# Kernel tuning notes

Hardware: AMD Instinct MI355X
Metric: run time of the kernel (lower is better)

Reference implementation:

```python
import jax, jax.numpy as jnp
import numpy as np

# Config constants (mirror Qwen3_5TextConfig)
H = 1024        # hidden_size
I = 512         # moe_intermediate_size
IS = 2048       # shared_expert_intermediate_size
E = 16          # num_experts
TOP_K = 4       # num_experts_per_tok
NORM_TOPK = True
B, S = 1, 1024


def setup_inputs() -> dict:
    key = jax.random.key(0)
    ks = jax.random.split(key, 10)
    s = 0.02
    return {
        "hidden_states": jax.random.normal(ks[0], (B, S, H), jnp.float32),
        "w_router": (jax.random.normal(ks[1], (H, E), jnp.float32) * s),
        # stacked expert weights; Linear(H->I) stored as [E, H, I] for einsum
        "w_gate": (jax.random.normal(ks[2], (E, H, I), jnp.float32) * s),
        "w_up": (jax.random.normal(ks[3], (E, H, I), jnp.float32) * s),
        "w_down": (jax.random.normal(ks[4], (E, I, H), jnp.float32) * s),
        # shared expert (dense MLP)
        "ws_gate": (jax.random.normal(ks[5], (H, IS), jnp.float32) * s),
        "ws_up": (jax.random.normal(ks[6], (H, IS), jnp.float32) * s),
        "ws_down": (jax.random.normal(ks[7], (IS, H), jnp.float32) * s),
        "w_shared_gate": (jax.random.normal(ks[8], (H, 1), jnp.float32) * s),
    }


def reference(hidden_states, w_router, w_gate, w_up, w_down,
              ws_gate, ws_up, ws_down, w_shared_gate):
    b, sl, hd = hidden_states.shape
    x = hidden_states.reshape(-1, hd)              # [T, H]
    T = x.shape[0]

    # --- router: softmax in fp32, top-k, optional renormalization ---
    router_logits = x @ w_router                   # [T, E]
    probs = jax.nn.softmax(router_logits.astype(jnp.float32), axis=-1)
    top_w, top_i = jax.lax.top_k(probs, TOP_K)     # [T, K]
    if NORM_TOPK:
        top_w = top_w / top_w.sum(axis=-1, keepdims=True)
    # dense per-token expert weights (zeros off the top-k)
    dense_w = jnp.zeros((T, E), x.dtype).at[jnp.arange(T)[:, None], top_i].set(
        top_w.astype(x.dtype))                     # [T, E]

    # --- expert MLPs (SwiGLU), computed for all experts then masked-combined ---
    g = jnp.einsum('th,ehi->tei', x, w_gate)       # [T, E, I]
    u = jnp.einsum('th,ehi->tei', x, w_up)         # [T, E, I]
    expert_out = jnp.einsum('tei,eih->teh', jax.nn.silu(g) * u, w_down)  # [T, E, H]
    moe_out = jnp.einsum('te,teh->th', dense_w, expert_out)             # [T, H]

    # --- shared expert + sigmoid gate ---
    shared = (jax.nn.silu(x @ ws_gate) * (x @ ws_up)) @ ws_down          # [T, H]
    shared_gate = jax.nn.sigmoid(x @ w_shared_gate)                      # [T, 1]
    out = (moe_out + shared_gate * shared).reshape(b, sl, hd)
    return out, router_logits
```

## Files before the change

### kernel.cpp

```cpp
#include <hip/hip_runtime.h>
#include <hip/hip_bf16.h>

#define T_ 1024
#define H_ 1024
#define I_ 512
#define IS_ 2048
#define E_ 16

typedef __attribute__((ext_vector_type(8))) short short8;
typedef __attribute__((ext_vector_type(4))) float f32x4;

__device__ __forceinline__ unsigned short f2bf(float f) {
  unsigned u = __builtin_bit_cast(unsigned, f);
  unsigned r = (u + 0x7fffu + ((u >> 16) & 1u)) >> 16;
  return (unsigned short)r;
}

__device__ __forceinline__ void gload16(const void* g, void* l) {
  __builtin_amdgcn_global_load_lds(
      (const __attribute__((address_space(1))) unsigned int*)g,
      (__attribute__((address_space(3))) unsigned int*)l, 16, 0, 0);
}

__device__ __forceinline__ void transpose_tile(
    const float* __restrict__ src, unsigned short* __restrict__ dst,
    int C, int dld, long sbs, long dbs, int bx, int by, int bz) {
  __shared__ unsigned short tile[64 * 72];
  const float* s = src + (long)bz * sbs + ((long)by * 64) * C + bx * 64;
  int cgrp = threadIdx.x & 15, rgrp = threadIdx.x >> 4;
  int c = cgrp << 2, r0 = rgrp << 2;
  const float* sp = s + (long)r0 * C + c;
  float4 v0 = *(const float4*)(sp);
  float4 v1 = *(const float4*)(sp + C);
  float4 v2 = *(const float4*)(sp + 2 * C);
  float4 v3 = *(const float4*)(sp + 3 * C);
  ushort4 w;
  w = (ushort4){f2bf(v0.x), f2bf(v1.x), f2bf(v2.x), f2bf(v3.x)};
  *(ushort4*)&tile[(c + 0) * 72 + r0] = w;
  w = (ushort4){f2bf(v0.y), f2bf(v1.y), f2bf(v2.y), f2bf(v3.y)};
  *(ushort4*)&tile[(c + 1) * 72 + r0] = w;
  w = (ushort4){f2bf(v0.z), f2bf(v1.z), f2bf(v2.z), f2bf(v3.z)};
  *(ushort4*)&tile[(c + 2) * 72 + r0] = w;
  w = (ushort4){f2bf(v0.w), f2bf(v1.w), f2bf(v2.w), f2bf(v3.w)};
  *(ushort4*)&tile[(c + 3) * 72 + r0] = w;
  __syncthreads();
  int orr = threadIdx.x >> 2;
  int ks = (threadIdx.x & 3) << 4;
  uint4 o0 = *(const uint4*)&tile[orr * 72 + ks];
  uint4 o1 = *(const uint4*)&tile[orr * 72 + ks + 8];
  unsigned short* d = dst + (long)bz * dbs + (long)(bx * 64 + orr) * dld + by * 64 + ks;
  *(uint4*)d = o0;
  *(uint4*)(d + 8) = o1;
}

__global__ __launch_bounds__(256) void k_pre(
    const float* __restrict__ x, const float* __restrict__ wr,
    const float* __restrict__ wshg,
    const float* __restrict__ wg, const float* __restrict__ wu,
    const float* __restrict__ wd, const float* __restrict__ wsg,
    const float* __restrict__ wsu, const float* __restrict__ wsd,
    unsigned short* __restrict__ xb, float* __restrict__ logits_out,
    int* __restrict__ top_i, float* __restrict__ top_w, float* __restrict__ gate_sig,
    unsigned short* __restrict__ WGUT, unsigned short* __restrict__ WDT,
    unsigned short* __restrict__ WSGUT, unsigned short* __restrict__ WSDT) {
  __shared__ float red[4][17];
  int id = blockIdx.x;
  if (id >= T_) {
    id -= T_;
    if (id < 4096) {
      const float* s = id < 2048 ? wg : wu;
      unsigned short* dd = id < 2048 ? WGUT : WGUT + (size_t)I_ * H_;
      int l = id & 2047;
      int bz = l >> 7, r = l & 127;
      transpose_tile(s, dd, I_, H_, (long)H_ * I_, (long)2 * I_ * H_, r & 7, r >> 3, bz);
    } else if (id < 6144) {
      int l = id - 4096;
      int bz = l >> 7, r = l & 127;
      transpose_tile(wd, WDT, H_, I_, (long)I_ * H_, (long)H_ * I_, r & 15, r >> 4, bz);
    } else if (id < 7168) {
      int l = id - 6144;
      const float* s = l < 512 ? wsg : wsu;
      unsigned short* dd = l < 512 ? WSGUT : WSGUT + (size_t)IS_ * H_;
      l &= 511;
      transpose_tile(s, dd, IS_, H_, 0, 0, l & 31, l >> 5, 0);
    } else {
      int l = id - 7168;
      transpose_tile(wsd, WSDT, H_, IS_, 0, 0, l & 15, l >> 4, 0);
    }
    return;
  }
  int t = id, tid = threadIdx.x;
  int h0 = tid << 2;
  float acc[17];
#pragma unroll
  for (int e = 0; e < 17; e++) acc[e] = 0.f;
  float4 xv = *(const float4*)(x + (long)t * H_ + h0);
  float4 wsh = *(const float4*)(wshg + h0);
  ushort4 xo;
  xo.x = f2bf(xv.x); xo.y = f2bf(xv.y); xo.z = f2bf(xv.z); xo.w = f2bf(xv.w);
  *(ushort4*)(xb + (long)t * H_ + h0) = xo;
  float xs[4] = {xv.x, xv.y, xv.z, xv.w};
  float ws[4] = {wsh.x, wsh.y, wsh.z, wsh.w};
#pragma unroll
  for (int j = 0; j < 4; j++) {
    const float4* w4 = (const float4*)(wr + (long)(h0 + j) * 16);
    float4 w0 = w4[0], w1 = w4[1], w2 = w4[2], w3 = w4[3];
    float xvj = xs[j];
    acc[0] += xvj * w0.x; acc[1] += xvj * w0.y; acc[2] += xvj * w0.z; acc[3] += xvj * w0.w;
    acc[4] += xvj * w1.x; acc[5] += xvj * w1.y; acc[6] += xvj * w1.z; acc[7] += xvj * w1.w;
    acc[8] += xvj * w2.x; acc[9] += xvj * w2.y; acc[10] += xvj * w2.z; acc[11] += xvj * w2.w;
    acc[12] += xvj * w3.x; acc[13] += xvj * w3.y; acc[14] += xvj * w3.z; acc[15] += xvj * w3.w;
    acc[16] += xvj * ws[j];
  }
#pragma unroll
  for (int off = 32; off >= 1; off >>= 1) {
#pragma unroll
    for (int e = 0; e < 17; e++) acc[e] += __shfl_xor(acc[e], off, 64);
  }
  int wid = tid >> 6, lane = tid & 63;
  if (lane == 0) {
#pragma unroll
    for (int e = 0; e < 17; e++) red[wid][e] = acc[e];
  }
  __syncthreads();
  if (tid == 0) {
    float a[17];
#pragma unroll
    for (int e = 0; e < 17; e++)
      a[e] = red[0][e] + red[1][e] + red[2][e] + red[3][e];
    float m = a[0];
#pragma unroll
    for (int e = 1; e < 16; e++) m = fmaxf(m, a[e]);
    float p[16], s = 0.f;
#pragma unroll
    for (int e = 0; e < 16; e++) { p[e] = expf(a[e] - m); s += p[e]; }
    float inv = 1.f / s;
#pragma unroll
    for (int e = 0; e < 16; e++) p[e] *= inv;
    int ti[4]; float tw[4]; float tsum = 0.f;
#pragma unroll
    for (int k = 0; k < 4; k++) {
      float best = -1.f; int bi = 0;
#pragma unroll
      for (int e = 0; e < 16; e++)
        if (p[e] > best) { best = p[e]; bi = e; }
      ti[k] = bi; tw[k] = best; tsum += best; p[bi] = -2.f;
    }
    float rn = 1.f / tsum;
#pragma unroll
    for (int e = 0; e < 16; e++) logits_out[(long)t * 16 + e] = a[e];
#pragma unroll
    for (int k = 0; k < 4; k++) {
      top_i[t * 4 + k] = ti[k];
      top_w[t * 4 + k] = tw[k] * rn;
    }
    gate_sig[t] = 1.f / (1.f + expf(-a[16]));
  }
}

__global__ __launch_bounds__(256) void k_build(
    const int* __restrict__ top_i, int* __restrict__ counts,
    int* __restrict__ offsets, int* __restrict__ perm, int* __restrict__ slot_of) {
  __shared__ int cnt[E_], cur[E_];
  int tid = threadIdx.x;
  if (tid < E_) cnt[tid] = 0;
  __syncthreads();
  for (int i = tid; i < T_ * 4; i += 256)
    atomicAdd(&cnt[top_i[i]], 1);
  __syncthreads();
  if (tid == 0) {
    int run = 0;
    for (int e = 0; e < E_; e++) {
      int c = cnt[e];
      counts[e] = c;
      offsets[e] = run;
      cur[e] = run;
      run += c;
    }
  }
  __syncthreads();
  for (int i = tid; i < T_ * 4; i += 256) {
    int e = top_i[i];
    int pos = atomicAdd(&cur[e], 1);
    perm[pos] = i >> 2;
    slot_of[i] = pos;
  }
}

__global__ __launch_bounds__(256) void k_gemm_gu(
    const unsigned short* __restrict__ XB,
    const unsigned short* __restrict__ WSGUT, const unsigned short* __restrict__ WGUT,
    unsigned short* __restrict__ HSB, unsigned short* __restrict__ HB,
    const int* __restrict__ counts, const int* __restrict__ offsets,
    const int* __restrict__ perm) {
  int z = blockIdx.z;
  int mtile = blockIdx.y * 64;
  int ntile = blockIdx.x * 128;
  int M, row_base, uoff, ldd;
  const unsigned short* B0;
  unsigned short* DST;
  const int* pp;
  if (z == 0) {
    M = T_; row_base = 0; B0 = WSGUT; uoff = IS_;
    DST = HSB; ldd = IS_; pp = nullptr;
  } else {
    if (ntile >= I_) return;
    int e = z - 1;
    M = counts[e];
    if (mtile >= M) return;
    row_base = offsets[e];
    B0 = WGUT + (long)e * 2 * I_ * H_;
    uoff = I_;
    DST = HB; ldd = I_; pp = perm;
  }

  __shared__ unsigned short lds[2][10240];

  int tid = threadIdx.x, wid = tid >> 6, lane = tid & 63;
  int sub = lane >> 2;
  int ksw = ((lane & 3) ^ ((sub >> 1) & 3)) << 3;

  int rm = mtile + wid * 16 + sub;
  if (rm > M - 1) rm = M - 1;
  long arow = pp ? (long)pp[row_base + rm] : (long)(row_base + rm);
  const unsigned short* aptr = XB + arow * H_ + ksw;
  int a_off = wid * 512;

  const unsigned short* bgptr[2];
  const unsigned short* buptr[2];
  int b_off[2];
#pragma unroll
  for (int q = 0; q < 2; q++) {
    int r = ntile + q * 64 + wid * 16 + sub;
    bgptr[q] = B0 + (long)r * H_ + ksw;
    buptr[q] = B0 + (long)(r + uoff) * H_ + ksw;
    b_off[q] = q * 2048 + wid * 512;
  }

  int fr = lane & 15, quad = lane >> 4;
  int fslot = (quad ^ ((fr >> 1) & 3)) << 3;
  int wm = (wid >> 1) * 32, wn = (wid & 1) * 64;

  f32x4 acc[2][2][4];
#pragma unroll
  for (int h = 0; h < 2; h++)
#pragma unroll
    for (int i = 0; i < 2; i++)
#pragma unroll
      for (int j = 0; j < 4; j++) acc[h][i][j] = (f32x4){0.f, 0.f, 0.f, 0.f};

  const int NK = H_ / 32;
  gload16(aptr, &lds[0][a_off]);
  gload16(bgptr[0], &lds[0][2048 + b_off[0]]);
  gload16(bgptr[1], &lds[0][2048 + b_off[1]]);
  gload16(buptr[0], &lds[0][6144 + b_off[0]]);
  gload16(buptr[1], &lds[0][6144 + b_off[1]]);

  for (int kt = 0; kt < NK; kt++) {
    int cur = kt & 1;
    __syncthreads();
    if (kt + 1 < NK) {
      int nxt = cur ^ 1, ko = (kt + 1) * 32;
      gload16(aptr + ko, &lds[nxt][a_off]);
      gload16(bgptr[0] + ko, &lds[nxt][2048 + b_off[0]]);
      gload16(bgptr[1] + ko, &lds[nxt][2048 + b_off[1]]);
      gload16(buptr[0] + ko, &lds[nxt][6144 + b_off[0]]);
      gload16(buptr[1] + ko, &lds[nxt][6144 + b_off[1]]);
    }
    const unsigned short* As = &lds[cur][0];
    const unsigned short* Bg = &lds[cur][2048];
    const unsigned short* Bu = &lds[cur][6144];
    short8 af[2], bg[4], bu[4];
#pragma unroll
    for (int i = 0; i < 2; i++)
      af[i] = *(const short8*)(&As[(wm + i * 16 + fr) * 32 + fslot]);
#pragma unroll
    for (int j = 0; j < 4; j++) {
      bg[j] = *(const short8*)(&Bg[(wn + j * 16 + fr) * 32 + fslot]);
      bu[j] = *(const short8*)(&Bu[(wn + j * 16 + fr) * 32 + fslot]);
    }
#pragma unroll
    for (int i = 0; i < 2; i++)
#pragma unroll
      for (int j = 0; j < 4; j++) {
        acc[0][i][j] = __builtin_amdgcn_mfma_f32_16x16x32_bf16(af[i], bg[j], acc[0][i][j], 0, 0, 0);
        acc[1][i][j] = __builtin_amdgcn_mfma_f32_16x16x32_bf16(af[i], bu[j], acc[1][i][j], 0, 0, 0);
      }
  }

#pragma unroll
  for (int i = 0; i < 2; i++) {
    int m0 = mtile + wm + i * 16 + quad * 4;
#pragma unroll
    for (int j = 0; j < 4; j++) {
      int col = ntile + wn + j * 16 + fr;
#pragma unroll
      for (int r = 0; r < 4; r++) {
        int m = m0 + r;
        if (m < M) {
          float g = acc[0][i][j][r], u = acc[1][i][j][r];
          DST[(long)(row_base + m) * ldd + col] = f2bf(g / (1.f + expf(-g)) * u);
        }
      }
    }
  }
}

__global__ __launch_bounds__(256) void k_gemm_dn(
    const unsigned short* __restrict__ HSB, const unsigned short* __restrict__ WSDT,
    float* __restrict__ SHOUT,
    const unsigned short* __restrict__ HB, const unsigned short* __restrict__ WDT,
    float* __restrict__ YD,
    const int* __restrict__ counts, const int* __restrict__ offsets) {
  int z = blockIdx.z;
  int mtile = blockIdx.y * 64;
  int ntile = blockIdx.x * 128;
  const unsigned short *A, *B;
  int K, M, rb;
  float* Y;
  if (z == 0) {
    A = HSB; K = IS_; M = T_; rb = 0; B = WSDT; Y = SHOUT;
  } else {
    int e = z - 1;
    M = counts[e];
    if (mtile >= M) return;
    rb = offsets[e];
    A = HB; K = I_; B = WDT + (long)e * H_ * I_; Y = YD;
  }

  __shared__ unsigned short lds[2][6144];

  int tid = threadIdx.x, wid = tid >> 6, lane = tid & 63;
  int sub = lane >> 2;
  int ksw = ((lane & 3) ^ ((sub >> 1) & 3)) << 3;

  int rm = mtile + wid * 16 + sub;
  if (rm > M - 1) rm = M - 1;
  const unsigned short* aptr = A + (long)(rb + rm) * K + ksw;
  int a_off = wid * 512;

  const unsigned short* bptr[2];
  int b_off[2];
#pragma unroll
  for (int q = 0; q < 2; q++) {
    int r = ntile + q * 64 + wid * 16 + sub;
    bptr[q] = B + (long)r * K + ksw;
    b_off[q] = q * 2048 + wid * 512;
  }

  int fr = lane & 15, quad = lane >> 4;
  int fslot = (quad ^ ((fr >> 1) & 3)) << 3;
  int wm = (wid >> 1) * 32, wn = (wid & 1) * 64;

  f32x4 acc[2][4];
#pragma unroll
  for (int i = 0; i < 2; i++)
#pragma unroll
    for (int j = 0; j < 4; j++) acc[i][j] = (f32x4){0.f, 0.f, 0.f, 0.f};

  const int NK = K / 32;
  gload16(aptr, &lds[0][a_off]);
  gload16(bptr[0], &lds[0][2048 + b_off[0]]);
  gload16(bptr[1], &lds[0][2048 + b_off[1]]);

  for (int kt = 0; kt < NK; kt++) {
    int cur = kt & 1;
    __syncthreads();
    if (kt + 1 < NK) {
      int nxt = cur ^ 1, ko = (kt + 1) * 32;
      gload16(aptr + ko, &lds[nxt][a_off]);
      gload16(bptr[0] + ko, &lds[nxt][2048 + b_off[0]]);
      gload16(bptr[1] + ko, &lds[nxt][2048 + b_off[1]]);
    }
    const unsigned short* As = &lds[cur][0];
    const unsigned short* Bs = &lds[cur][2048];
    short8 af[2], bf[4];
#pragma unroll
    for (int i = 0; i < 2; i++)
      af[i] = *(const short8*)(&As[(wm + i * 16 + fr) * 32 + fslot]);
#pragma unroll
    for (int j = 0; j < 4; j++)
      bf[j] = *(const short8*)(&Bs[(wn + j * 16 + fr) * 32 + fslot]);
#pragma unroll
    for (int i = 0; i < 2; i++)
#pragma unroll
      for (int j = 0; j < 4; j++)
        acc[i][j] = __builtin_amdgcn_mfma_f32_16x16x32_bf16(af[i], bf[j], acc[i][j], 0, 0, 0);
  }

#pragma unroll
  for (int i = 0; i < 2; i++) {
    int m0 = mtile + wm + i * 16 + quad * 4;
#pragma unroll
    for (int j = 0; j < 4; j++) {
      int col = ntile + wn + j * 16 + fr;
#pragma unroll
      for (int r = 0; r < 4; r++) {
        int m = m0 + r;
        if (m < M) Y[(long)(rb + m) * H_ + col] = acc[i][j][r];
      }
    }
  }
}

__global__ __launch_bounds__(256) void k_combine(
    const float* __restrict__ Yd, const float* __restrict__ shout,
    const float* __restrict__ gate_sig, const float* __restrict__ top_w,
    const int* __restrict__ slot_of, float* __restrict__ out) {
  int t = blockIdx.x;
  int c = threadIdx.x << 2;
  float4 sh = *(const float4*)(shout + (long)t * H_ + c);
  float gs = gate_sig[t];
  float4 o;
  o.x = gs * sh.x; o.y = gs * sh.y; o.z = gs * sh.z; o.w = gs * sh.w;
#pragma unroll
  for (int k = 0; k < 4; k++) {
    int s = slot_of[t * 4 + k];
    float w = top_w[t * 4 + k];
    float4 v = *(const float4*)(Yd + (long)s * H_ + c);
    o.x += w * v.x; o.y += w * v.y; o.z += w * v.z; o.w += w * v.w;
  }
  *(float4*)(out + (long)t * H_ + c) = o;
}

extern "C" void kernel_launch(void* const* d_in, const int* in_sizes, int n_in,
                              void* d_out, int out_size, void* d_ws, size_t ws_size,
                              hipStream_t stream) {
  const float* x    = (const float*)d_in[0];
  const float* wrt  = (const float*)d_in[1];
  const float* wg   = (const float*)d_in[2];
  const float* wu   = (const float*)d_in[3];
  const float* wd   = (const float*)d_in[4];
  const float* wsg  = (const float*)d_in[5];
  const float* wsu  = (const float*)d_in[6];
  const float* wsd  = (const float*)d_in[7];
  const float* wshg = (const float*)d_in[8];
  float* out = (float*)d_out;
  float* logits_out = out + (long)T_ * H_;

  char* ws = (char*)d_ws;
  size_t off = 0;
  auto take = [&](size_t bytes) -> void* {
    void* p = ws + off;
    off += (bytes + 255) & ~(size_t)255;
    return p;
  };

  unsigned short* XB    = (unsigned short*)take((size_t)T_ * H_ * 2);
  unsigned short* WGUT  = (unsigned short*)take((size_t)E_ * 2 * I_ * H_ * 2);
  unsigned short* WDT   = (unsigned short*)take((size_t)E_ * H_ * I_ * 2);
  unsigned short* WSGUT = (unsigned short*)take((size_t)2 * IS_ * H_ * 2);
  unsigned short* WSDT  = (unsigned short*)take((size_t)H_ * IS_ * 2);
  float*          YD    = (float*)take((size_t)4096 * H_ * 4);
  unsigned short* HSB   = (unsigned short*)take((size_t)T_ * IS_ * 2);
  float*          SHOUT = (float*)take((size_t)T_ * H_ * 4);
  unsigned short* HB    = (unsigned short*)take((size_t)4096 * I_ * 2);
  int*   counts   = (int*)take(64);
  int*   offsets  = (int*)take(64);
  int*   top_i    = (int*)take((size_t)T_ * 4 * 4);
  float* top_w    = (float*)take((size_t)T_ * 4 * 4);
  int*   perm     = (int*)take((size_t)4096 * 4);
  int*   slot_of  = (int*)take((size_t)4096 * 4);
  float* gate_sig = (float*)take((size_t)T_ * 4);

  k_pre<<<8704, 256, 0, stream>>>(x, wrt, wshg, wg, wu, wd, wsg, wsu, wsd,
                                  XB, logits_out, top_i, top_w, gate_sig,
                                  WGUT, WDT, WSGUT, WSDT);
  k_build<<<1, 256, 0, stream>>>(top_i, counts, offsets, perm, slot_of);

  k_gemm_gu<<<dim3(16, 16, 17), 256, 0, stream>>>(XB, WSGUT, WGUT, HSB, HB,
                                                  counts, offsets, perm);
  k_gemm_dn<<<dim3(8, 16, 17), 256, 0, stream>>>(HSB, WSDT, SHOUT, HB, WDT, YD,
                                                 counts, offsets);
  k_combine<<<T_, 256, 0, stream>>>(YD, SHOUT, gate_sig, top_w, slot_of, out);
}
```

Measured before the change: 287.9 us.

## Halve GEMM N-tile to 64 and use explicit waitcnt/barrier pipelining

```diff
diff --git a/kernel.cpp b/kernel.cpp
--- a/kernel.cpp
+++ b/kernel.cpp
@@ -195,7 +195,7 @@
     const int* __restrict__ perm) {
   int z = blockIdx.z;
   int mtile = blockIdx.y * 64;
-  int ntile = blockIdx.x * 128;
+  int ntile = blockIdx.x * 64;
   int M, row_base, uoff, ldd;
   const unsigned short* B0;
   unsigned short* DST;
@@ -214,7 +214,7 @@
     DST = HB; ldd = I_; pp = perm;
   }
 
-  __shared__ unsigned short lds[2][10240];
+  __shared__ unsigned short lds[2][6144];
 
   int tid = threadIdx.x, wid = tid >> 6, lane = tid & 63;
   int sub = lane >> 2;
@@ -224,75 +224,70 @@
   if (rm > M - 1) rm = M - 1;
   long arow = pp ? (long)pp[row_base + rm] : (long)(row_base + rm);
   const unsigned short* aptr = XB + arow * H_ + ksw;
-  int a_off = wid * 512;
-
-  const unsigned short* bgptr[2];
-  const unsigned short* buptr[2];
-  int b_off[2];
-#pragma unroll
-  for (int q = 0; q < 2; q++) {
-    int r = ntile + q * 64 + wid * 16 + sub;
-    bgptr[q] = B0 + (long)r * H_ + ksw;
-    buptr[q] = B0 + (long)(r + uoff) * H_ + ksw;
-    b_off[q] = q * 2048 + wid * 512;
-  }
+  int rbn = ntile + wid * 16 + sub;
+  const unsigned short* bgptr = B0 + (long)rbn * H_ + ksw;
+  const unsigned short* buptr = B0 + (long)(rbn + uoff) * H_ + ksw;
+  int soff = wid * 512;
 
   int fr = lane & 15, quad = lane >> 4;
   int fslot = (quad ^ ((fr >> 1) & 3)) << 3;
-  int wm = (wid >> 1) * 32, wn = (wid & 1) * 64;
-
-  f32x4 acc[2][2][4];
+  int wm = (wid >> 1) * 32, wn = (wid & 1) * 32;
+
+  f32x4 acc[2][2][2];
 #pragma unroll
   for (int h = 0; h < 2; h++)
 #pragma unroll
     for (int i = 0; i < 2; i++)
 #pragma unroll
-      for (int j = 0; j < 4; j++) acc[h][i][j] = (f32x4){0.f, 0.f, 0.f, 0.f};
+      for (int j = 0; j < 2; j++) acc[h][i][j] = (f32x4){0.f, 0.f, 0.f, 0.f};
 
   const int NK = H_ / 32;
-  gload16(aptr, &lds[0][a_off]);
-  gload16(bgptr[0], &lds[0][2048 + b_off[0]]);
-  gload16(bgptr[1], &lds[0][2048 + b_off[1]]);
-  gload16(buptr[0], &lds[0][6144 + b_off[0]]);
-  gload16(buptr[1], &lds[0][6144 + b_off[1]]);
+  gload16(aptr, &lds[0][soff]);
+  gload16(bgptr, &lds[0][2048 + soff]);
+  gload16(buptr, &lds[0][4096 + soff]);
 
   for (int kt = 0; kt < NK; kt++) {
     int cur = kt & 1;
-    __syncthreads();
     if (kt + 1 < NK) {
-      int nxt = cur ^ 1, ko = (kt + 1) * 32;
-      gload16(aptr + ko, &lds[nxt][a_off]);
-      gload16(bgptr[0] + ko, &lds[nxt][2048 + b_off[0]]);
-      gload16(bgptr[1] + ko, &lds[nxt][2048 + b_off[1]]);
-      gload16(buptr[0] + ko, &lds[nxt][6144 + b_off[0]]);
-      gload16(buptr[1] + ko, &lds[nxt][6144 + b_off[1]]);
-    }
+      int ko = (kt + 1) * 32;
+      gload16(aptr + ko, &lds[cur ^ 1][soff]);
+      gload16(bgptr + ko, &lds[cur ^ 1][2048 + soff]);
+      gload16(buptr + ko, &lds[cur ^ 1][4096 + soff]);
+      asm volatile("s_waitcnt vmcnt(3)" ::: "memory");
+    } else {
+      asm volatile("s_waitcnt vmcnt(0)" ::: "memory");
+    }
+    __builtin_amdgcn_s_barrier();
+    __builtin_amdgcn_sched_barrier(0);
     const unsigned short* As = &lds[cur][0];
     const unsigned short* Bg = &lds[cur][2048];
-    const unsigned short* Bu = &lds[cur][6144];
-    short8 af[2], bg[4], bu[4];
+    const unsigned short* Bu = &lds[cur][4096];
+    short8 af[2], bg[2], bu[2];
 #pragma unroll
     for (int i = 0; i < 2; i++)
       af[i] = *(const short8*)(&As[(wm + i * 16 + fr) * 32 + fslot]);
 #pragma unroll
-    for (int j = 0; j < 4; j++) {
+    for (int j = 0; j < 2; j++) {
       bg[j] = *(const short8*)(&Bg[(wn + j * 16 + fr) * 32 + fslot]);
       bu[j] = *(const short8*)(&Bu[(wn + j * 16 + fr) * 32 + fslot]);
     }
 #pragma unroll
     for (int i = 0; i < 2; i++)
 #pragma unroll
-      for (int j = 0; j < 4; j++) {
+      for (int j = 0; j < 2; j++) {
         acc[0][i][j] = __builtin_amdgcn_mfma_f32_16x16x32_bf16(af[i], bg[j], acc[0][i][j], 0, 0, 0);
         acc[1][i][j] = __builtin_amdgcn_mfma_f32_16x16x32_bf16(af[i], bu[j], acc[1][i][j], 0, 0, 0);
       }
+    asm volatile("s_waitcnt lgkmcnt(0)" ::: "memory");
+    __builtin_amdgcn_sched_barrier(0);
+    __builtin_amdgcn_s_barrier();
   }
 
 #pragma unroll
   for (int i = 0; i < 2; i++) {
     int m0 = mtile + wm + i * 16 + quad * 4;
 #pragma unroll
-    for (int j = 0; j < 4; j++) {
+    for (int j = 0; j < 2; j++) {
       int col = ntile + wn + j * 16 + fr;
 #pragma unroll
       for (int r = 0; r < 4; r++) {
@@ -314,7 +309,7 @@
     const int* __restrict__ counts, const int* __restrict__ offsets) {
   int z = blockIdx.z;
   int mtile = blockIdx.y * 64;
-  int ntile = blockIdx.x * 128;
+  int ntile = blockIdx.x * 64;
   const unsigned short *A, *B;
   int K, M, rb;
   float* Y;
@@ -328,7 +323,7 @@
     A = HB; K = I_; B = WDT + (long)e * H_ * I_; Y = YD;
   }
 
-  __shared__ unsigned short lds[2][6144];
+  __shared__ unsigned short lds[2][4096];
 
   int tid = threadIdx.x, wid = tid >> 6, lane = tid & 63;
   int sub = lane >> 2;
@@ -337,62 +332,60 @@
   int rm = mtile + wid * 16 + sub;
   if (rm > M - 1) rm = M - 1;
   const unsigned short* aptr = A + (long)(rb + rm) * K + ksw;
-  int a_off = wid * 512;
-
-  const unsigned short* bptr[2];
-  int b_off[2];
-#pragma unroll
-  for (int q = 0; q < 2; q++) {
-    int r = ntile + q * 64 + wid * 16 + sub;
-    bptr[q] = B + (long)r * K + ksw;
-    b_off[q] = q * 2048 + wid * 512;
-  }
+  int rbn = ntile + wid * 16 + sub;
+  const unsigned short* bptr = B + (long)rbn * K + ksw;
+  int soff = wid * 512;
 
   int fr = lane & 15, quad = lane >> 4;
   int fslot = (quad ^ ((fr >> 1) & 3)) << 3;
-  int wm = (wid >> 1) * 32, wn = (wid & 1) * 64;
-
-  f32x4 acc[2][4];
+  int wm = (wid >> 1) * 32, wn = (wid & 1) * 32;
+
+  f32x4 acc[2][2];
 #pragma unroll
   for (int i = 0; i < 2; i++)
 #pragma unroll
-    for (int j = 0; j < 4; j++) acc[i][j] = (f32x4){0.f, 0.f, 0.f, 0.f};
+    for (int j = 0; j < 2; j++) acc[i][j] = (f32x4){0.f, 0.f, 0.f, 0.f};
 
   const int NK = K / 32;
-  gload16(aptr, &lds[0][a_off]);
-  gload16(bptr[0], &lds[0][2048 + b_off[0]]);
-  gload16(bptr[1], &lds[0][2048 + b_off[1]]);
+  gload16(aptr, &lds[0][soff]);
+  gload16(bptr, &lds[0][2048 + soff]);
 
   for (int kt = 0; kt < NK; kt++) {
     int cur = kt & 1;
-    __syncthreads();
     if (kt + 1 < NK) {
-      int nxt = cur ^ 1, ko = (kt + 1) * 32;
-      gload16(aptr + ko, &lds[nxt][a_off]);
-      gload16(bptr[0] + ko, &lds[nxt][2048 + b_off[0]]);
-      gload16(bptr[1] + ko, &lds[nxt][2048 + b_off[1]]);
-    }
+      int ko = (kt + 1) * 32;
+      gload16(aptr + ko, &lds[cur ^ 1][soff]);
+      gload16(bptr + ko, &lds[cur ^ 1][2048 + soff]);
+      asm volatile("s_waitcnt vmcnt(2)" ::: "memory");
+    } else {
+      asm volatile("s_waitcnt vmcnt(0)" ::: "memory");
+    }
+    __builtin_amdgcn_s_barrier();
+    __builtin_amdgcn_sched_barrier(0);
     const unsigned short* As = &lds[cur][0];
     const unsigned short* Bs = &lds[cur][2048];
-    short8 af[2], bf[4];
+    short8 af[2], bf[2];
 #pragma unroll
     for (int i = 0; i < 2; i++)
       af[i] = *(const short8*)(&As[(wm + i * 16 + fr) * 32 + fslot]);
 #pragma unroll
-    for (int j = 0; j < 4; j++)
+    for (int j = 0; j < 2; j++)
       bf[j] = *(const short8*)(&Bs[(wn + j * 16 + fr) * 32 + fslot]);
 #pragma unroll
     for (int i = 0; i < 2; i++)
 #pragma unroll
-      for (int j = 0; j < 4; j++)
+      for (int j = 0; j < 2; j++)
         acc[i][j] = __builtin_amdgcn_mfma_f32_16x16x32_bf16(af[i], bf[j], acc[i][j], 0, 0, 0);
+    asm volatile("s_waitcnt lgkmcnt(0)" ::: "memory");
+    __builtin_amdgcn_sched_barrier(0);
+    __builtin_amdgcn_s_barrier();
   }
 
 #pragma unroll
   for (int i = 0; i < 2; i++) {
     int m0 = mtile + wm + i * 16 + quad * 4;
 #pragma unroll
-    for (int j = 0; j < 4; j++) {
+    for (int j = 0; j < 2; j++) {
       int col = ntile + wn + j * 16 + fr;
 #pragma unroll
       for (int r = 0; r < 4; r++) {
@@ -468,9 +461,9 @@
                                   WGUT, WDT, WSGUT, WSDT);
   k_build<<<1, 256, 0, stream>>>(top_i, counts, offsets, perm, slot_of);
 
-  k_gemm_gu<<<dim3(16, 16, 17), 256, 0, stream>>>(XB, WSGUT, WGUT, HSB, HB,
+  k_gemm_gu<<<dim3(32, 16, 17), 256, 0, stream>>>(XB, WSGUT, WGUT, HSB, HB,
                                                   counts, offsets, perm);
-  k_gemm_dn<<<dim3(8, 16, 17), 256, 0, stream>>>(HSB, WSDT, SHOUT, HB, WDT, YD,
-                                                 counts, offsets);
+  k_gemm_dn<<<dim3(16, 16, 17), 256, 0, stream>>>(HSB, WSDT, SHOUT, HB, WDT, YD,
+                                                  counts, offsets);
   k_combine<<<T_, 256, 0, stream>>>(YD, SHOUT, gate_sig, top_w, slot_of, out);
 }
```

Result: faster. 279.7 us (-2.9%).
